# Kernel tuning notes

Hardware: AMD Instinct MI355X
Metric: run time of the kernel (lower is better)

## Reference

```python
import jax, jax.numpy as jnp
import numpy as np

N, E, IN, OUT, R, B = 20000, 640000, 128, 128, 64, 16


def setup_inputs() -> dict:
    key = jax.random.key(0)
    ks = jax.random.split(key, 9)
    xav_w = float(np.sqrt(2.0 / (IN + OUT)))  # xavier-uniform-ish scale
    xav_c = float(np.sqrt(2.0 / (R + B)))
    return {
        "x": jax.random.normal(ks[0], (N, IN), jnp.float32),
        "weight": jax.random.normal(ks[1], (B, IN, OUT), jnp.float32) * xav_w,
        "w_comp": jax.random.normal(ks[2], (R, B), jnp.float32) * xav_c,
        "h_bias": jnp.zeros((OUT,), jnp.float32),
        "loop_weight": jax.random.normal(ks[3], (IN, OUT), jnp.float32) * xav_w,
        "norm": jax.random.uniform(ks[4], (E, 1), jnp.float32),
        "src": jax.random.randint(ks[5], (E,), 0, N, jnp.int32),
        "dst": jax.random.randint(ks[6], (E,), 0, N, jnp.int32),
        "etypes": jax.random.randint(ks[7], (E,), 0, R, jnp.int32),
    }


def reference(x, weight, w_comp, h_bias, loop_weight, norm, src, dst, etypes):
    # Basis composition: per-relation weights W_rel[r] = sum_b w_comp[r,b] * weight[b]
    W_rel = jnp.einsum("rb,bio->rio", w_comp, weight)          # [R, IN, OUT]
    # Project every node through every relation weight (N*R << per-edge bmm
    # of E gathered [IN,OUT] matrices; same math as bmm_maybe_select).
    h_all = jnp.einsum("ni,rio->nro", x, W_rel)                 # [N, R, OUT]
    # Per-edge message: msg_e = x[src_e] @ W_rel[etype_e], scaled by norm
    msg = h_all[src, etypes] * norm                              # [E, OUT]
    # fn.sum aggregation to destination nodes
    agg = jax.ops.segment_sum(msg, dst, num_segments=x.shape[0])  # [N, OUT]
    out = agg + h_bias + x @ loop_weight                          # bias + self-loop
    return jax.nn.relu(out)                                       # activation; dropout p=0
```

## Files before the change

### kernel.cpp

```cpp
#include <hip/hip_runtime.h>

#define N_NODES 20000
#define E_EDGES 640000
#define R_REL   64
#define B_BASES 16
#define NSEG    128
#define SEGLEN  (E_EDGES / NSEG)
#define RH      10000
#define NBPR    32
#define QG      ((2 * NSEG) / 16)

#define PB_WREL (R_REL * 16)
#define PB_LW   (PB_WREL + 16)
#define PB_XH   (PB_LW + 2500)
#define PB_HIST (PB_XH + 2 * NSEG)

#define SELF_B  ((N_NODES + 63) / 64)

typedef __attribute__((ext_vector_type(4))) float f32x4;
typedef __attribute__((ext_vector_type(8))) _Float16 half8;

__device__ inline float h2f(unsigned short v) {
    _Float16 h; __builtin_memcpy(&h, &v, 2); return (float)h;
}
__device__ inline unsigned short f2h(float f) {
    _Float16 h = (_Float16)f; unsigned short v; __builtin_memcpy(&v, &h, 2); return v;
}

__device__ inline void gld_lds16(const void* g, void* l) {
    __builtin_amdgcn_global_load_lds(
        (const __attribute__((address_space(1))) void*)g,
        (__attribute__((address_space(3))) void*)l, 16, 0, 0);
}

__global__ void k_prep(const float* weight, const float* w_comp, unsigned short* wt_h,
                       const float* lw, unsigned short* lwT,
                       const float* x, unsigned short* xh,
                       const int* etypes, const int* dst,
                       unsigned short* hps, int* he)
{
    __shared__ float tile[32][33];
    __shared__ float wcS[B_BASES];
    __shared__ int lh[RH];
    __shared__ int heL[R_REL];
    int b = blockIdx.x, t = threadIdx.x;
    int tx = t & 31, ty = t >> 5;

    if (b < PB_WREL) {
        int r  = b >> 4;
        int ti = (b >> 2) & 3;
        int tj = b & 3;
        if (t < B_BASES) wcS[t] = w_comp[r * B_BASES + t];
        __syncthreads();
        float acc[4] = {0.f, 0.f, 0.f, 0.f};
        const float* wp = weight + (ti * 32) * 128 + tj * 32;
        for (int bb = 0; bb < B_BASES; bb++) {
            float c = wcS[bb];
            #pragma unroll
            for (int s = 0; s < 4; s++)
                acc[s] += c * wp[bb * 16384 + (ty + s * 8) * 128 + tx];
        }
        #pragma unroll
        for (int s = 0; s < 4; s++) tile[ty + s * 8][tx] = acc[s];
        __syncthreads();
        unsigned short* dstp = wt_h + r * 16384 + (tj * 32) * 128 + ti * 32;
        #pragma unroll
        for (int s = 0; s < 4; s++)
            dstp[(ty + s * 8) * 128 + tx] = f2h(tile[tx][ty + s * 8]);
        return;
    }
    if (b < PB_LW) {
        int q = b - PB_WREL;
        int ti = q >> 2, tj = q & 3;
        const float* srcp = lw + (ti * 32) * 128 + tj * 32;
        #pragma unroll
        for (int s = 0; s < 4; s++)
            tile[ty + s * 8][tx] = srcp[(ty + s * 8) * 128 + tx];
        __syncthreads();
        unsigned short* d = lwT + (tj * 32) * 128 + ti * 32;
        #pragma unroll
        for (int s = 0; s < 4; s++)
            d[(ty + s * 8) * 128 + tx] = f2h(tile[tx][ty + s * 8]);
        return;
    }
    if (b < PB_XH) {
        int i4 = (b - PB_LW) * 256 + t;
        float4 v = ((const float4*)x)[i4];
        ushort4 o;
        o.x = f2h(v.x); o.y = f2h(v.y); o.z = f2h(v.z); o.w = f2h(v.w);
        ((ushort4*)xh)[i4] = o;
        return;
    }
    {
        int q = b - PB_XH;
        int s = q >> 1, h = q & 1;
        for (int i = t; i < RH; i += 256) lh[i] = 0;
        if (t < R_REL) heL[t] = 0;
        __syncthreads();
        int e0 = s * SEGLEN;
        for (int k = t; k < SEGLEN; k += 256) {
            int e = e0 + k;
            int d = dst[e];
            unsigned ld = (unsigned)(d - h * RH);
            if (ld < RH) {
                atomicAdd(&lh[ld], 1);
                atomicAdd(&heL[etypes[e]], 1);
            }
        }
        __syncthreads();
        for (int i = t; i < RH; i += 256)
            hps[(size_t)s * N_NODES + h * RH + i] = (unsigned short)lh[i];
        if (t < R_REL) he[q * 64 + t] = heL[t];
    }
}

__global__ void k_sumc(const unsigned short* hps, int* counts2)
{
    int n = blockIdx.x * 256 + threadIdx.x;
    if (n >= N_NODES) return;
    int s = 0;
    for (int q = 0; q < NSEG; q += 8) {
        int v[8];
        #pragma unroll
        for (int k = 0; k < 8; k++) v[k] = hps[(size_t)(q + k) * N_NODES + n];
        #pragma unroll
        for (int k = 0; k < 8; k++) s += v[k];
    }
    counts2[n] = s;
}

__global__ void k_segbase(unsigned short* hps)
{
    int n = blockIdx.x * 256 + threadIdx.x;
    if (n >= N_NODES) return;
    int run = 0;
    for (int q = 0; q < NSEG; q += 8) {
        int v[8];
        #pragma unroll
        for (int k = 0; k < 8; k++) v[k] = hps[(size_t)(q + k) * N_NODES + n];
        #pragma unroll
        for (int k = 0; k < 8; k++) {
            hps[(size_t)(q + k) * N_NODES + n] = (unsigned short)run;
            run += v[k];
        }
    }
}

__global__ void k_scan_all2(const int* he, const int* counts2,
                            int* offsets, int* off2, int* be)
{
    __shared__ int part[1024];
    __shared__ int psum[16][R_REL];
    __shared__ int offL[R_REL];
    int tid = threadIdx.x;
    int t = tid & 63;
    int g = tid >> 6;
    int vals[QG];
    int ps = 0;
    #pragma unroll
    for (int k = 0; k < QG; k++) {
        vals[k] = he[(g * QG + k) * 64 + t];
        ps += vals[k];
    }
    psum[g][t] = ps;
    __syncthreads();
    if (tid < 64) {
        int c = 0;
        #pragma unroll
        for (int gg = 0; gg < 16; gg++) c += psum[gg][t];
        int s1 = c;
        for (int d = 1; d < 64; d <<= 1) {
            int a1 = __shfl_up(s1, d);
            if (t >= d) s1 += a1;
        }
        offsets[t] = s1 - c;
        offL[t] = s1 - c;
        if (t == 63) offsets[64] = s1;
    }
    __syncthreads();
    {
        int run = offL[t];
        for (int gg = 0; gg < g; gg++) run += psum[gg][t];
        #pragma unroll
        for (int k = 0; k < QG; k++) {
            be[(g * QG + k) * 64 + t] = run;
            run += vals[k];
        }
    }
    int lo_i = tid * 20, hi_i = lo_i + 20;
    if (hi_i > N_NODES) hi_i = N_NODES;
    if (lo_i > N_NODES) lo_i = N_NODES;
    int s = 0;
    for (int i = lo_i; i < hi_i; i++) s += counts2[i];
    part[tid] = s;
    __syncthreads();
    for (int d = 1; d < 1024; d <<= 1) {
        int v = (tid >= d) ? part[tid - d] : 0;
        __syncthreads();
        part[tid] += v;
        __syncthreads();
    }
    int run = part[tid] - s;
    for (int i = lo_i; i < hi_i; i++) {
        off2[i] = run;
        run += counts2[i];
    }
    if (tid == 1023) off2[N_NODES] = run;
}

__global__ void k_scatter3(const int* etypes, const int* dst, const int* src, const float* norm,
                           const unsigned short* hps, const int* be, const int* off2,
                           int* perm_src, float* pnorm, int* pos2)
{
    __shared__ int lbase[RH];
    __shared__ int ebase[R_REL];
    int t = threadIdx.x, q = blockIdx.x;
    int s = q >> 1, h = q & 1;
    for (int i = t; i < RH; i += 256)
        lbase[i] = off2[h * RH + i] + (int)hps[(size_t)s * N_NODES + h * RH + i];
    if (t < R_REL) ebase[t] = be[q * 64 + t];
    __syncthreads();
    int e0 = s * SEGLEN;
    for (int k = t; k < SEGLEN; k += 256) {
        int e = e0 + k;
        int d = dst[e];
        unsigned ld = (unsigned)(d - h * RH);
        if (ld < RH) {
            int slot = atomicAdd(&lbase[ld], 1);
            int p = atomicAdd(&ebase[etypes[e]], 1);
            perm_src[p] = src[e];
            pnorm[p] = norm[e];
            pos2[p] = slot;
        }
    }
}

__global__ __launch_bounds__(256) void k_edge_mfma(
    const unsigned short* __restrict__ xh, const unsigned short* __restrict__ wt_h,
    const unsigned short* __restrict__ lwT,
    const int* __restrict__ perm_src, const float* __restrict__ pnorm,
    const int* __restrict__ pos2, const int* __restrict__ offsets,
    unsigned short* __restrict__ msg, float* __restrict__ out)
{
    __shared__ __align__(16) char smemW[32768];
    int t = threadIdx.x, b = blockIdx.x;
    int l = t & 63, w = t >> 6;
    int lg = l >> 4, lr = l & 15;
    const half8* smW = (const half8*)smemW;

    if (b >= R_REL * NBPR) {
        int n0 = (b - R_REL * NBPR) * 64;
        #pragma unroll
        for (int it = 0; it < 8; it++) {
            int s = it * 256 + t;
            int o = s >> 4, ch = s & 15;
            int jx = ch ^ (o & 15);
            gld_lds16(lwT + o * 128 + jx * 8, smemW + s * 16);
        }
        int rowA = w * 16 + lr;
        int nA = n0 + rowA; if (nA >= N_NODES) nA = N_NODES - 1;
        const half8* xr = (const half8*)(xh + (size_t)nA * 128);
        half8 avC[4];
        #pragma unroll
        for (int kk = 0; kk < 4; kk++) avC[kk] = xr[kk * 4 + lg];
        f32x4 acc[8];
        #pragma unroll
        for (int n = 0; n < 8; n++) acc[n] = {0.0f, 0.0f, 0.0f, 0.0f};
        __syncthreads();
        #pragma unroll
        for (int kk = 0; kk < 4; kk++) {
            #pragma unroll
            for (int n = 0; n < 8; n++) {
                int o = n * 16 + lr;
                half8 bv = smW[o * 16 + ((kk * 4 + lg) ^ (o & 15))];
                acc[n] = __builtin_amdgcn_mfma_f32_16x16x32_f16(avC[kk], bv, acc[n], 0, 0, 0);
            }
        }
        #pragma unroll
        for (int jj = 0; jj < 4; jj++) {
            int row = w * 16 + lg * 4 + jj;
            int n = n0 + row;
            if (n < N_NODES) {
                float4 v0, v1;
                v0.x = acc[0][jj]; v0.y = acc[1][jj]; v0.z = acc[2][jj]; v0.w = acc[3][jj];
                v1.x = acc[4][jj]; v1.y = acc[5][jj]; v1.z = acc[6][jj]; v1.w = acc[7][jj];
                *(float4*)(out + (size_t)n * 128 + lr * 8) = v0;
                *(float4*)(out + (size_t)n * 128 + lr * 8 + 4) = v1;
            }
        }
        return;
    }

    int r = b >> 5;
    int j = b & (NBPR - 1);
    int p0 = offsets[r], p1 = offsets[r + 1];
    int nch = (p1 - p0 + 63) >> 6;

    {
        const size_t rbase = (size_t)r * 16384;
        #pragma unroll
        for (int it = 0; it < 8; it++) {
            int s = it * 256 + t;
            int o = s >> 4, ch = s & 15;
            int jx = ch ^ (o & 15);
            gld_lds16(wt_h + rbase + o * 128 + jx * 8, smemW + s * 16);
        }
    }

    int rowA = w * 16 + lr;

    int i = j;
    int sN = 0;
    if (i < nch) {
        int e0 = p0 + i * 64;
        int cnt = p1 - e0; if (cnt > 64) cnt = 64;
        sN = (rowA < cnt) ? perm_src[e0 + rowA] : 0;
    }

    __syncthreads();

    half8 avC[4];
    {
        const half8* xr = (const half8*)(xh + (size_t)sN * 128);
        #pragma unroll
        for (int kk = 0; kk < 4; kk++) avC[kk] = xr[kk * 4 + lg];
    }
    int i2 = i + NBPR;
    if (i2 < nch) {
        int e0 = p0 + i2 * 64;
        int cnt = p1 - e0; if (cnt > 64) cnt = 64;
        sN = (rowA < cnt) ? perm_src[e0 + rowA] : 0;
    }

    while (i < nch) {
        int e0 = p0 + i * 64;
        int cnt = p1 - e0; if (cnt > 64) cnt = 64;

        int slotC[4]; float nrmC[4];
        #pragma unroll
        for (int jj = 0; jj < 4; jj++) {
            int row = w * 16 + lg * 4 + jj;
            bool vld = row < cnt;
            slotC[jj] = vld ? pos2[e0 + row] : -1;
            nrmC[jj]  = vld ? pnorm[e0 + row] : 0.0f;
        }

        half8 avN[4];
        {
            const half8* xr = (const half8*)(xh + (size_t)sN * 128);
            #pragma unroll
            for (int kk = 0; kk < 4; kk++) avN[kk] = xr[kk * 4 + lg];
        }
        int i3 = i2 + NBPR;
        if (i3 < nch) {
            int e0n = p0 + i3 * 64;
            int cntn = p1 - e0n; if (cntn > 64) cntn = 64;
            sN = (rowA < cntn) ? perm_src[e0n + rowA] : 0;
        }

        f32x4 acc[8];
        #pragma unroll
        for (int n = 0; n < 8; n++) acc[n] = {0.0f, 0.0f, 0.0f, 0.0f};

        #pragma unroll
        for (int kk = 0; kk < 4; kk++) {
            #pragma unroll
            for (int n = 0; n < 8; n++) {
                int o = n * 16 + lr;
                half8 bv = smW[o * 16 + ((kk * 4 + lg) ^ (o & 15))];
                acc[n] = __builtin_amdgcn_mfma_f32_16x16x32_f16(avC[kk], bv, acc[n], 0, 0, 0);
            }
        }

        #pragma unroll
        for (int jj = 0; jj < 4; jj++) {
            int slot = slotC[jj];
            if (slot >= 0) {
                float nm = nrmC[jj];
                uint4 ov;
                ov.x = (unsigned int)f2h(acc[0][jj] * nm) | ((unsigned int)f2h(acc[1][jj] * nm) << 16);
                ov.y = (unsigned int)f2h(acc[2][jj] * nm) | ((unsigned int)f2h(acc[3][jj] * nm) << 16);
                ov.z = (unsigned int)f2h(acc[4][jj] * nm) | ((unsigned int)f2h(acc[5][jj] * nm) << 16);
                ov.w = (unsigned int)f2h(acc[6][jj] * nm) | ((unsigned int)f2h(acc[7][jj] * nm) << 16);
                *(uint4*)(msg + (size_t)slot * 128 + lr * 8) = ov;
            }
        }

        #pragma unroll
        for (int kk = 0; kk < 4; kk++) avC[kk] = avN[kk];
        i = i2; i2 = i3;
    }
}

__global__ void k_msgsum(const unsigned short* msg, const int* off2,
                         const float* bias, float* out)
{
    __shared__ float4 red[256];
    __shared__ float fin[128];
    int n = blockIdx.x, t = threadIdx.x;
    int m0 = off2[n], m1 = off2[n + 1];
    int rp = t >> 5, c = t & 31;
    float4 a; a.x = 0.f; a.y = 0.f; a.z = 0.f; a.w = 0.f;
    for (int j = m0 + rp; j < m1; j += 8) {
        uint2 v = *(const uint2*)(msg + (size_t)j * 128 + c * 4);
        a.x += h2f((unsigned short)(v.x & 0xffff));
        a.y += h2f((unsigned short)(v.x >> 16));
        a.z += h2f((unsigned short)(v.y & 0xffff));
        a.w += h2f((unsigned short)(v.y >> 16));
    }
    red[t] = a;
    __syncthreads();
    if (t < 128) {
        float4 b = red[t + 128];
        red[t].x += b.x; red[t].y += b.y; red[t].z += b.z; red[t].w += b.w;
    }
    __syncthreads();
    if (t < 64) {
        float4 b = red[t + 64];
        red[t].x += b.x; red[t].y += b.y; red[t].z += b.z; red[t].w += b.w;
    }
    __syncthreads();
    if (t < 32) {
        float4 v = red[t], b = red[t + 32];
        v.x += b.x; v.y += b.y; v.z += b.z; v.w += b.w;
        float4 o = *(const float4*)(out + (size_t)n * 128 + t * 4);
        v.x += o.x; v.y += o.y; v.z += o.z; v.w += o.w;
        int base = (t & 1) * 64 + (t >> 1);
        fin[base]      = v.x;
        fin[base + 16] = v.y;
        fin[base + 32] = v.z;
        fin[base + 48] = v.w;
    }
    __syncthreads();
    if (t < 32) {
        float4 f = ((const float4*)fin)[t];
        float4 bb = *(const float4*)(bias + t * 4);
        f.x += bb.x; f.y += bb.y; f.z += bb.z; f.w += bb.w;
        if (f.x < 0.f) f.x = 0.f;
        if (f.y < 0.f) f.y = 0.f;
        if (f.z < 0.f) f.z = 0.f;
        if (f.w < 0.f) f.w = 0.f;
        *(float4*)(out + (size_t)n * 128 + t * 4) = f;
    }
}


__global__ void k_wrel(const float* weight, const float* w_comp, float* W_rel)
{
    int idx = blockIdx.x * 256 + threadIdx.x;
    int r  = idx >> 14;
    int io = idx & 16383;
    float acc = 0.0f;
    for (int b = 0; b < B_BASES; b++)
        acc += w_comp[r * B_BASES + b] * weight[b * 16384 + io];
    W_rel[idx] = acc;
}

__global__ void k_zero(float* agg, int* counts, int* counts2)
{
    int idx = blockIdx.x * 256 + threadIdx.x;
    if (idx < N_NODES * 128) agg[idx] = 0.0f;
    if (idx < R_REL) counts[idx] = 0;
    if (idx < N_NODES) counts2[idx] = 0;
}

__global__ void k_hist(const int* etypes, int* counts)
{
    __shared__ int h[R_REL];
    int t = threadIdx.x;
    if (t < R_REL) h[t] = 0;
    __syncthreads();
    int e = blockIdx.x * 256 + t;
    atomicAdd(&h[etypes[e]], 1);
    __syncthreads();
    if (t < R_REL && h[t] != 0) atomicAdd(&counts[t], h[t]);
}

__global__ void k_scan(const int* counts, int* offsets, int* cursor, int* co)
{
    if (threadIdx.x == 0) {
        int run = 0, c = 0;
        for (int r = 0; r < R_REL; r++) {
            offsets[r] = run; cursor[r] = run; co[r] = c;
            run += counts[r];
            c   += (counts[r] + 63) >> 6;
        }
        offsets[R_REL] = run; co[R_REL] = c;
    }
}

__global__ void k_scatter(const int* etypes, int* cursor, int* perm)
{
    __shared__ int h[R_REL];
    __shared__ int base[R_REL];
    int t = threadIdx.x;
    if (t < R_REL) h[t] = 0;
    __syncthreads();
    int e = blockIdx.x * 256 + t;
    int et = etypes[e];
    int rank = atomicAdd(&h[et], 1);
    __syncthreads();
    if (t < R_REL && h[t] != 0) base[t] = atomicAdd(&cursor[t], h[t]);
    __syncthreads();
    perm[base[et] + rank] = e;
}

__global__ void k_edge_atomic(const float* x, const float* W_rel, const float* norm,
                              const int* src, const int* dst, const int* perm,
                              const int* offsets, const int* co, float* agg)
{
    __shared__ float4 WfS[2048];
    __shared__ float4 xsS[1024];
    __shared__ int coS[R_REL + 1];
    __shared__ int srcS[64], dstS[64];
    __shared__ float normS[64];
    int t = threadIdx.x, bid = blockIdx.x;
    if (t <= R_REL) coS[t] = co[t];
    __syncthreads();
    if (bid >= coS[R_REL]) return;
    int r = 0;
    while (bid >= coS[r + 1]) r++;
    int e0 = offsets[r] + (bid - coS[r]) * 64;
    int cnt = offsets[r + 1] - e0;
    if (cnt > 64) cnt = 64;
    if (t < 64) {
        if (t < cnt) {
            int eid = perm[e0 + t];
            srcS[t] = src[eid]; dstS[t] = dst[eid]; normS[t] = norm[eid];
        } else { srcS[t] = 0; dstS[t] = 0; normS[t] = 0.0f; }
    }
    const float* xsf = (const float*)xsS;
    int q  = t & 31;
    int eb = t >> 5;
    float4 acc[8];
    for (int k = 0; k < 8; k++) { acc[k].x = 0.f; acc[k].y = 0.f; acc[k].z = 0.f; acc[k].w = 0.f; }
    for (int h = 0; h < 2; h++) {
        __syncthreads();
        const float4* Wsrc = (const float4*)(W_rel + r * 16384 + h * 8192);
        for (int p = 0; p < 8; p++) WfS[p * 256 + t] = Wsrc[p * 256 + t];
        for (int p = 0; p < 4; p++) {
            int idx = p * 256 + t;
            int e = idx >> 4, c = idx & 15;
            xsS[idx] = ((const float4*)(x + srcS[e] * 128 + h * 64))[c];
        }
        __syncthreads();
        for (int i = 0; i < 64; i++) {
            float4 wv = WfS[i * 32 + q];
            for (int k = 0; k < 8; k++) {
                float xv = xsf[(eb + 8 * k) * 64 + i];
                acc[k].x += xv * wv.x;
                acc[k].y += xv * wv.y;
                acc[k].z += xv * wv.z;
                acc[k].w += xv * wv.w;
            }
        }
    }
    for (int k = 0; k < 8; k++) {
        int e = eb + 8 * k;
        if (e < cnt) {
            float nrm = normS[e];
            float* row = agg + dstS[e] * 128 + q * 4;
            atomicAdd(row + 0, acc[k].x * nrm);
            atomicAdd(row + 1, acc[k].y * nrm);
            atomicAdd(row + 2, acc[k].z * nrm);
            atomicAdd(row + 3, acc[k].w * nrm);
        }
    }
}

__global__ void k_out(const float* x, const float* loop_w, const float* agg,
                      const float* bias, float* out)
{
    __shared__ float xrow[128];
    int n = blockIdx.x;
    int o = threadIdx.x;
    xrow[o] = x[n * 128 + o];
    __syncthreads();
    float acc = 0.0f;
    for (int i = 0; i < 128; i++)
        acc += xrow[i] * loop_w[i * 128 + o];
    float val = acc + agg[n * 128 + o] + bias[o];
    if (val < 0.0f) val = 0.0f;
    out[n * 128 + o] = val;
}

extern "C" void kernel_launch(void* const* d_in, const int* in_sizes, int n_in,
                              void* d_out, int out_size, void* d_ws, size_t ws_size,
                              hipStream_t stream)
{
    const float* x      = (const float*)d_in[0];
    const float* weight = (const float*)d_in[1];
    const float* w_comp = (const float*)d_in[2];
    const float* h_bias = (const float*)d_in[3];
    const float* loop_w = (const float*)d_in[4];
    const float* norm   = (const float*)d_in[5];
    const int* src    = (const int*)d_in[6];
    const int* dst    = (const int*)d_in[7];
    const int* etypes = (const int*)d_in[8];
    float* out = (float*)d_out;

    char* ws = (char*)d_ws;
    size_t off = 0;
    float* W_rel = (float*)(ws + off); off += (size_t)R_REL * 16384 * 4;
    float* agg   = (float*)(ws + off); off += (size_t)N_NODES * 128 * 4;
    int* perm    = (int*)(ws + off);   off += (size_t)E_EDGES * 4;
    int* counts  = (int*)(ws + off);   off += 64 * 4;
    int* offsets = (int*)(ws + off);   off += 68 * 4;
    int* cursor  = (int*)(ws + off);   off += 64 * 4;
    int* co      = (int*)(ws + off);   off += 68 * 4;
    int* counts2 = (int*)(ws + off);   off += (size_t)N_NODES * 4;
    int* off2    = (int*)(ws + off);   off += (size_t)(N_NODES + 4) * 4;
    int* cursor2 = (int*)(ws + off);   off += (size_t)N_NODES * 4;
    int* pos2    = (int*)(ws + off);   off += (size_t)E_EDGES * 4;
    unsigned short* msg = (unsigned short*)(ws + off);
    size_t need_big = off + (size_t)E_EDGES * 128 * 2;
    int big = (ws_size >= need_big) ? 1 : 0;

    if (big) {
        unsigned short* wt_h = (unsigned short*)W_rel;
        char* wspare = (char*)W_rel + (size_t)2 * 1024 * 1024;
        unsigned short* lwT = (unsigned short*)wspare;
        unsigned short* xh = (unsigned short*)agg;
        float* pnorm = (float*)((char*)agg + (size_t)N_NODES * 128 * 2);
        int* perm_src = perm;
        unsigned short* hps = (unsigned short*)msg;
        int* he = (int*)((char*)msg + (size_t)NSEG * N_NODES * 2);
        int* be = (int*)((char*)he + (size_t)2 * NSEG * 64 * 4);

        k_prep<<<PB_HIST, 256, 0, stream>>>(weight, w_comp, wt_h, loop_w, lwT,
                                            x, xh, etypes, dst, hps, he);
        k_sumc<<<(N_NODES + 255) / 256, 256, 0, stream>>>(hps, counts2);
        k_segbase<<<(N_NODES + 255) / 256, 256, 0, stream>>>(hps);
        k_scan_all2<<<1, 1024, 0, stream>>>(he, counts2, offsets, off2, be);
        k_scatter3<<<2 * NSEG, 256, 0, stream>>>(etypes, dst, src, norm,
                                                 hps, be, off2, perm_src, pnorm, pos2);
        k_edge_mfma<<<R_REL * NBPR + SELF_B, 256, 0, stream>>>(
            xh, wt_h, lwT, perm_src, pnorm, pos2, offsets, msg, out);
        k_msgsum<<<N_NODES, 256, 0, stream>>>(msg, off2, h_bias, out);
    } else {
        k_wrel<<<(R_REL * 16384) / 256, 256, 0, stream>>>(weight, w_comp, W_rel);
        k_zero<<<(N_NODES * 128) / 256, 256, 0, stream>>>(agg, counts, counts2);
        k_hist<<<E_EDGES / 256, 256, 0, stream>>>(etypes, counts);
        k_scan<<<1, 64, 0, stream>>>(counts, offsets, cursor, co);
        k_scatter<<<E_EDGES / 256, 256, 0, stream>>>(etypes, cursor, perm);
        k_edge_atomic<<<E_EDGES / 64 + R_REL, 256, 0, stream>>>(
            x, W_rel, norm, src, dst, perm, offsets, co, agg);
        k_out<<<N_NODES, 128, 0, stream>>>(x, loop_w, agg, h_bias, out);
    }
}
```

Baseline: 268.7 us.

## Fuse count kernels, double edge blocks per relation, use wave-per-node message sum

Merges the per-node count summation and the segment-base prefix into one kernel, saving a launch and a second pass over the histogram. Doubles the number of edge GEMM blocks per relation for more parallelism. Rewrites the message aggregation so each wavefront handles one node with no shared-memory reductions or barriers, processing four messages per loop iteration. The per-node loop now runs serially within a wave, so high-degree nodes take longer, and the new output column permutation must match the old layout exactly.

```diff
diff --git a/kernel.cpp b/kernel.cpp
--- a/kernel.cpp
+++ b/kernel.cpp
@@ -7,7 +7,7 @@
 #define NSEG    128
 #define SEGLEN  (E_EDGES / NSEG)
 #define RH      10000
-#define NBPR    32
+#define NBPR    64
 #define QG      ((2 * NSEG) / 16)
 
 #define PB_WREL (R_REL * 16)
@@ -114,22 +114,7 @@
     }
 }
 
-__global__ void k_sumc(const unsigned short* hps, int* counts2)
-{
-    int n = blockIdx.x * 256 + threadIdx.x;
-    if (n >= N_NODES) return;
-    int s = 0;
-    for (int q = 0; q < NSEG; q += 8) {
-        int v[8];
-        #pragma unroll
-        for (int k = 0; k < 8; k++) v[k] = hps[(size_t)(q + k) * N_NODES + n];
-        #pragma unroll
-        for (int k = 0; k < 8; k++) s += v[k];
-    }
-    counts2[n] = s;
-}
-
-__global__ void k_segbase(unsigned short* hps)
+__global__ void k_sumseg(unsigned short* hps, int* counts2)
 {
     int n = blockIdx.x * 256 + threadIdx.x;
     if (n >= N_NODES) return;
@@ -144,6 +129,7 @@
             run += v[k];
         }
     }
+    counts2[n] = run;
 }
 
 __global__ void k_scan_all2(const int* he, const int* counts2,
@@ -291,7 +277,7 @@
         return;
     }
 
-    int r = b >> 5;
+    int r = b >> 6;
     int j = b & (NBPR - 1);
     int p0 = offsets[r], p1 = offsets[r + 1];
     int nch = (p1 - p0 + 63) >> 6;
@@ -392,56 +378,42 @@
     }
 }
 
-__global__ void k_msgsum(const unsigned short* msg, const int* off2,
-                         const float* bias, float* out)
-{
-    __shared__ float4 red[256];
-    __shared__ float fin[128];
-    int n = blockIdx.x, t = threadIdx.x;
+__global__ __launch_bounds__(256) void k_msgsum(const unsigned short* __restrict__ msg,
+                                                const int* __restrict__ off2,
+                                                const float* __restrict__ bias,
+                                                float* __restrict__ out)
+{
+    int t = threadIdx.x;
+    int wv = t >> 6, c = t & 63;
+    int n = blockIdx.x * 4 + wv;
+    if (n >= N_NODES) return;
     int m0 = off2[n], m1 = off2[n + 1];
-    int rp = t >> 5, c = t & 31;
-    float4 a; a.x = 0.f; a.y = 0.f; a.z = 0.f; a.w = 0.f;
-    for (int j = m0 + rp; j < m1; j += 8) {
-        uint2 v = *(const uint2*)(msg + (size_t)j * 128 + c * 4);
-        a.x += h2f((unsigned short)(v.x & 0xffff));
-        a.y += h2f((unsigned short)(v.x >> 16));
-        a.z += h2f((unsigned short)(v.y & 0xffff));
-        a.w += h2f((unsigned short)(v.y >> 16));
-    }
-    red[t] = a;
-    __syncthreads();
-    if (t < 128) {
-        float4 b = red[t + 128];
-        red[t].x += b.x; red[t].y += b.y; red[t].z += b.z; red[t].w += b.w;
-    }
-    __syncthreads();
-    if (t < 64) {
-        float4 b = red[t + 64];
-        red[t].x += b.x; red[t].y += b.y; red[t].z += b.z; red[t].w += b.w;
-    }
-    __syncthreads();
-    if (t < 32) {
-        float4 v = red[t], b = red[t + 32];
-        v.x += b.x; v.y += b.y; v.z += b.z; v.w += b.w;
-        float4 o = *(const float4*)(out + (size_t)n * 128 + t * 4);
-        v.x += o.x; v.y += o.y; v.z += o.z; v.w += o.w;
-        int base = (t & 1) * 64 + (t >> 1);
-        fin[base]      = v.x;
-        fin[base + 16] = v.y;
-        fin[base + 32] = v.z;
-        fin[base + 48] = v.w;
-    }
-    __syncthreads();
-    if (t < 32) {
-        float4 f = ((const float4*)fin)[t];
-        float4 bb = *(const float4*)(bias + t * 4);
-        f.x += bb.x; f.y += bb.y; f.z += bb.z; f.w += bb.w;
-        if (f.x < 0.f) f.x = 0.f;
-        if (f.y < 0.f) f.y = 0.f;
-        if (f.z < 0.f) f.z = 0.f;
-        if (f.w < 0.f) f.w = 0.f;
-        *(float4*)(out + (size_t)n * 128 + t * 4) = f;
-    }
+    float a0 = 0.0f, a1 = 0.0f;
+    int j = m0;
+    for (; j + 4 <= m1; j += 4) {
+        unsigned v0 = *(const unsigned*)(msg + (size_t)(j + 0) * 128 + c * 2);
+        unsigned v1 = *(const unsigned*)(msg + (size_t)(j + 1) * 128 + c * 2);
+        unsigned v2 = *(const unsigned*)(msg + (size_t)(j + 2) * 128 + c * 2);
+        unsigned v3 = *(const unsigned*)(msg + (size_t)(j + 3) * 128 + c * 2);
+        a0 += h2f((unsigned short)(v0 & 0xffff)) + h2f((unsigned short)(v1 & 0xffff))
+            + h2f((unsigned short)(v2 & 0xffff)) + h2f((unsigned short)(v3 & 0xffff));
+        a1 += h2f((unsigned short)(v0 >> 16)) + h2f((unsigned short)(v1 >> 16))
+            + h2f((unsigned short)(v2 >> 16)) + h2f((unsigned short)(v3 >> 16));
+    }
+    for (; j < m1; j++) {
+        unsigned v = *(const unsigned*)(msg + (size_t)j * 128 + c * 2);
+        a0 += h2f((unsigned short)(v & 0xffff));
+        a1 += h2f((unsigned short)(v >> 16));
+    }
+    float2 o = *(const float2*)(out + (size_t)n * 128 + c * 2);
+    a0 += o.x; a1 += o.y;
+    int cp0 = c * 2;
+    int nc0 = (cp0 & 7) * 16 + (cp0 >> 3);
+    a0 += bias[nc0]; a1 += bias[nc0 + 16];
+    if (a0 < 0.0f) a0 = 0.0f;
+    if (a1 < 0.0f) a1 = 0.0f;
+    out[(size_t)n * 128 + nc0]      = a0;
+    out[(size_t)n * 128 + nc0 + 16] = a1;
 }
 
 
@@ -629,14 +601,13 @@
 
         k_prep<<<PB_HIST, 256, 0, stream>>>(weight, w_comp, wt_h, loop_w, lwT,
                                             x, xh, etypes, dst, hps, he);
-        k_sumc<<<(N_NODES + 255) / 256, 256, 0, stream>>>(hps, counts2);
-        k_segbase<<<(N_NODES + 255) / 256, 256, 0, stream>>>(hps);
+        k_sumseg<<<(N_NODES + 255) / 256, 256, 0, stream>>>(hps, counts2);
         k_scan_all2<<<1, 1024, 0, stream>>>(he, counts2, offsets, off2, be);
         k_scatter3<<<2 * NSEG, 256, 0, stream>>>(etypes, dst, src, norm,
                                                  hps, be, off2, perm_src, pnorm, pos2);
         k_edge_mfma<<<R_REL * NBPR + SELF_B, 256, 0, stream>>>(
             xh, wt_h, lwT, perm_src, pnorm, pos2, offsets, msg, out);
-        k_msgsum<<<N_NODES, 256, 0, stream>>>(msg, off2, h_bias, out);
+        k_msgsum<<<(N_NODES + 3) / 4, 256, 0, stream>>>(msg, off2, h_bias, out);
     } else {
         k_wrel<<<(R_REL * 16384) / 256, 256, 0, stream>>>(weight, w_comp, W_rel);
         k_zero<<<(N_NODES * 128) / 256, 256, 0, stream>>>(agg, counts, counts2);
```

After: 258.0 us. 4.0% less time.
